# Kernel optimization log

Measured on AMD Instinct MI355X. Metric: run time of the kernel, lower is better.

The kernel has to match this reference:

```python
import jax, jax.numpy as jnp
import numpy as np

N = 50000      # nodes
E = 800000     # directed edges (avg degree 16 in/out pairs)
F_IN = 16      # dataset.num_features
H = 64         # neuron
S = 7          # Chebyshev order


def setup_inputs() -> dict:
    key = jax.random.key(0)
    ks = jax.random.split(key, 12)
    x = jax.random.normal(ks[0], (N, F_IN), dtype=jnp.float32)
    row = jax.random.randint(ks[1], (E,), 0, N, dtype=jnp.int32)
    off = jax.random.randint(ks[2], (E,), 1, N, dtype=jnp.int32)
    col = (row + off) % N  # guarantees no self-loops (PyG removes them)
    edge_index = jnp.stack([row, col])
    lambda_max = jnp.array([2.0], dtype=jnp.float32)
    def lin(k, fi, fo):
        return jax.random.normal(k, (S, fi, fo), dtype=jnp.float32) * (1.0 / np.sqrt(fi))
    W1 = lin(ks[3], F_IN, H); b1 = jnp.zeros((H,), jnp.float32)
    W2 = lin(ks[4], H, H);    b2 = jnp.zeros((H,), jnp.float32)
    W3 = lin(ks[5], H, H);    b3 = jnp.zeros((H,), jnp.float32)
    Wfc = jax.random.normal(ks[6], (H, 1), dtype=jnp.float32) * (1.0 / np.sqrt(H))
    bfc = jnp.zeros((1,), jnp.float32)
    return {"x": x, "edge_index": edge_index, "lambda_max": lambda_max,
            "W1": W1, "b1": b1, "W2": W2, "b2": b2, "W3": W3, "b3": b3,
            "Wfc": Wfc, "bfc": bfc}


def _make_spmv(edge_index, lam, n):
    # L_hat = 2/lambda_max * (I - D^-1/2 A D^-1/2) - I  (PyG ChebConv sym norm)
    row, col = edge_index[0], edge_index[1]
    deg = jax.ops.segment_sum(jnp.ones_like(row, dtype=jnp.float32), row, num_segments=n)
    dis = jnp.where(deg > 0, jax.lax.rsqrt(jnp.maximum(deg, 1.0)), 0.0)
    w = -(2.0 / lam) * dis[row] * dis[col]      # off-diagonal edge weights
    diag = 2.0 / lam - 1.0                       # self-loop weight
    def spmv(xx):  # L_hat @ xx
        return jax.ops.segment_sum(w[:, None] * xx[col], row, num_segments=n) + diag * xx
    return spmv


def _cheb(xx, W, b, spmv):
    Tx0 = xx
    out = Tx0 @ W[0]
    Tx1 = spmv(Tx0)
    out = out + Tx1 @ W[1]
    for k in range(2, W.shape[0]):  # fixed small S loop
        Tx2 = 2.0 * spmv(Tx1) - Tx0
        out = out + Tx2 @ W[k]
        Tx0, Tx1 = Tx1, Tx2
    return out + b


def reference(x, edge_index, lambda_max, W1, b1, W2, b2, W3, b3, Wfc, bfc):
    lam = lambda_max[0]
    spmv = _make_spmv(edge_index, lam, x.shape[0])
    h = jax.nn.relu(_cheb(x, W1, b1, spmv))
    h = jax.nn.relu(_cheb(h, W2, b2, spmv))
    h = jax.nn.relu(_cheb(h, W3, b3, spmv))
    return h @ Wfc + bfc
```

## Files before the change

### kernel.cpp

```cpp
#include <hip/hip_runtime.h>
#include <math.h>


#define WS_ALIGN(x) (((size_t)(x) + 255) & ~(size_t)255)

using f16x8 = __attribute__((ext_vector_type(8))) _Float16;
using f32x4 = __attribute__((ext_vector_type(4))) float;

__device__ inline float h2f_bits(unsigned int b) {
  unsigned short s = (unsigned short)(b & 0xffffu);
  _Float16 h;
  __builtin_memcpy(&h, &s, 2);
  return (float)h;
}
__device__ inline unsigned short f2h_bits(float f) {
  _Float16 h = (_Float16)f;
  unsigned short s;
  __builtin_memcpy(&s, &h, 2);
  return s;
}
union H4 {
  ushort4 u;
  _Float16 h[4];
};

__global__ __launch_bounds__(256) void hist_kernel(const int* __restrict__ row, int E,
                                                   int* __restrict__ deg) {
  int i = blockIdx.x * 256 + threadIdx.x;
  if (i < E) atomicAdd(&deg[row[i]], 1);
}

__global__ __launch_bounds__(256) void scan_sum_kernel(const int* __restrict__ deg,
                                                       int* __restrict__ bsum, int n) {
  int base = blockIdx.x * 1024 + threadIdx.x;
  int v = 0;
#pragma unroll
  for (int u = 0; u < 4; ++u) {
    int i = base + u * 256;
    if (i < n) v += deg[i];
  }
#pragma unroll
  for (int off = 32; off > 0; off >>= 1) v += __shfl_down(v, off, 64);
  __shared__ int ws[4];
  int lane = threadIdx.x & 63, wave = threadIdx.x >> 6;
  if (lane == 0) ws[wave] = v;
  __syncthreads();
  if (threadIdx.x == 0) bsum[blockIdx.x] = ws[0] + ws[1] + ws[2] + ws[3];
}

__global__ __launch_bounds__(64) void scan_bsum_kernel(int* __restrict__ bsum, int nb) {
  int t = threadIdx.x;
  int v = (t < nb) ? bsum[t] : 0;
  int sc = v;
#pragma unroll
  for (int off = 1; off < 64; off <<= 1) {
    int tv = __shfl_up(sc, off, 64);
    if (t >= off) sc += tv;
  }
  if (t < nb) bsum[t] = sc - v;
}

__global__ __launch_bounds__(256) void scan_out_kernel(const int* __restrict__ deg,
                                                       const int* __restrict__ bsum,
                                                       int* __restrict__ row_ptr,
                                                       int* __restrict__ cursor,
                                                       float* __restrict__ dis, int n) {
  int base = blockIdx.x * 1024 + threadIdx.x * 4;
  int loc[4];
  int s = 0;
#pragma unroll
  for (int u = 0; u < 4; ++u) {
    int i = base + u;
    loc[u] = (i < n) ? deg[i] : 0;
    s += loc[u];
  }
  int lane = threadIdx.x & 63, wave = threadIdx.x >> 6;
  int sc = s;
#pragma unroll
  for (int off = 1; off < 64; off <<= 1) {
    int tv = __shfl_up(sc, off, 64);
    if (lane >= off) sc += tv;
  }
  __shared__ int wtot[4];
  if (lane == 63) wtot[wave] = sc;
  __syncthreads();
  int pre = sc - s + bsum[blockIdx.x];
  for (int w = 0; w < wave; ++w) pre += wtot[w];
  if (blockIdx.x == 0 && threadIdx.x == 0) row_ptr[0] = 0;
  int running = pre;
#pragma unroll
  for (int u = 0; u < 4; ++u) {
    int i = base + u;
    if (i < n) {
      cursor[i] = running;
      dis[i] = (loc[u] > 0) ? (1.0f / sqrtf((float)loc[u])) : 0.0f;
      running += loc[u];
      row_ptr[i + 1] = running;
    }
  }
}

__global__ __launch_bounds__(256) void scatter_kernel(const int* __restrict__ row,
                                                      const int* __restrict__ col, int E,
                                                      int* __restrict__ cursor,
                                                      const float* __restrict__ dis,
                                                      const float* __restrict__ lamp,
                                                      unsigned int* __restrict__ cw) {
  int i = blockIdx.x * 256 + threadIdx.x;
  if (i >= E) return;
  int r = row[i], c = col[i];
  int pos = atomicAdd(&cursor[r], 1);
  float w = -(2.0f / lamp[0]) * dis[r] * dis[c];
  cw[pos] = ((unsigned int)c << 16) | (unsigned int)f2h_bits(w);
}

__global__ __launch_bounds__(256) void x_to_t1_kernel(const float* __restrict__ x,
                                                      ushort* __restrict__ T1, int n) {
  int j = blockIdx.x * 256 + threadIdx.x;
  if (j >= n * 8) return;
  int row = j >> 3, s = j & 7;
  if (s < 4) {
    float4 v = ((const float4*)x)[(size_t)row * 4 + s];
    ushort4 o;
    o.x = f2h_bits(v.x);
    o.y = f2h_bits(v.y);
    o.z = f2h_bits(v.z);
    o.w = f2h_bits(v.w);
    ((ushort4*)T1)[(size_t)row * 32 + s] = o;
  } else {
    ((ushort4*)T1)[(size_t)row * 32 + 28 + (s - 4)] = make_ushort4(0, 0, 0, 0);
  }
}

template <int KREAL, int KT>
__global__ __launch_bounds__(256) void wpk_prep(const float* __restrict__ W,
                                                ushort* __restrict__ Wpk) {
  int t = blockIdx.x * 256 + threadIdx.x;
  if (t >= KT * 256) return;
  int kt = t >> 8, nt = (t >> 6) & 3, l = t & 63;
  int col = nt * 16 + (l & 15);
  int kb = kt * 32 + ((l >> 4) << 3);
  ushort tmp[8];
#pragma unroll
  for (int j = 0; j < 8; ++j) {
    int k = kb + j;
    float v = (k < KREAL) ? W[(size_t)k * 64 + col] : 0.0f;
    tmp[j] = f2h_bits(v);
  }
  ushort4* dst = (ushort4*)Wpk + (size_t)((kt * 4 + nt) * 64 + l) * 2;
  dst[0] = make_ushort4(tmp[0], tmp[1], tmp[2], tmp[3]);
  dst[1] = make_ushort4(tmp[4], tmp[5], tmp[6], tmp[7]);
}

template <int F, int MODE, int S4>
__global__ __launch_bounds__(256) void spmv_pure(const int* __restrict__ row_ptr,
                                                 const unsigned int* __restrict__ cw,
                                                 const float* __restrict__ lamp,
                                                 const ushort4* __restrict__ xin,
                                                 const ushort4* __restrict__ sub,
                                                 ushort4* __restrict__ xout, int n) {
  constexpr int LPR = F / 4;
  constexpr int RPB = 256 / LPR;
  constexpr int EPL = 16 / LPR;
  int i = blockIdx.x * RPB + threadIdx.y;
  if (i >= n) return;
  int f4 = threadIdx.x;
  int lane = (threadIdx.y * LPR + f4) & 63;
  int grpbase = lane - f4;
  float diag = 2.0f / lamp[0] - 1.0f;
  H4 xd;
  xd.u = xin[(size_t)i * S4 + f4];
  float4 a = make_float4(diag * (float)xd.h[0], diag * (float)xd.h[1],
                         diag * (float)xd.h[2], diag * (float)xd.h[3]);
  int s = row_ptr[i], e = row_ptr[i + 1];

  for (int j0 = s; j0 < e; j0 += 16) {
    unsigned int pv[EPL];
#pragma unroll
    for (int u = 0; u < EPL; ++u) {
      int jj = j0 + f4 * EPL + u;
      pv[u] = cw[jj < e ? jj : (e - 1)];
    }
    H4 xv[16];
    float ww[16];
#pragma unroll
    for (int u = 0; u < 16; ++u) {
      unsigned int pu = (unsigned int)__shfl((int)pv[u % EPL], grpbase + u / EPL, 64);
      bool valid = (j0 + u) < e;
      ww[u] = valid ? h2f_bits(pu) : 0.0f;
      int ad = valid ? (int)(pu >> 16) : i;
      xv[u].u = xin[(size_t)ad * S4 + f4];
    }
#pragma unroll
    for (int u = 0; u < 16; ++u) {
      a.x += ww[u] * (float)xv[u].h[0];
      a.y += ww[u] * (float)xv[u].h[1];
      a.z += ww[u] * (float)xv[u].h[2];
      a.w += ww[u] * (float)xv[u].h[3];
    }
  }

  float4 r;
  if (MODE == 1) {
    H4 sv;
    sv.u = sub[(size_t)i * S4 + f4];
    r = make_float4(2.0f * a.x - (float)sv.h[0], 2.0f * a.y - (float)sv.h[1],
                    2.0f * a.z - (float)sv.h[2], 2.0f * a.w - (float)sv.h[3]);
  } else {
    r = a;
  }
  ushort4 o;
  o.x = f2h_bits(r.x);
  o.y = f2h_bits(r.y);
  o.z = f2h_bits(r.z);
  o.w = f2h_bits(r.w);
  xout[(size_t)i * S4 + f4] = o;
}

template <int KT, bool LAST>
__global__ __launch_bounds__(256) void gemm_mfma(const ushort* __restrict__ A,
                                                 const ushort* __restrict__ Wpk,
                                                 const float* __restrict__ bias,
                                                 ushort* __restrict__ dsth, int dstride,
                                                 float* __restrict__ dacc, int n) {
  int l = threadIdx.x & 63;
  int tile = blockIdx.x * 4 + (threadIdx.x >> 6);
  int r0 = tile * 16;
  if (r0 >= n) return;
  constexpr int ASTR = KT * 32;
  const f16x8* ap = (const f16x8*)(A + (size_t)(r0 + (l & 15)) * ASTR + ((l >> 4) << 3));
  const f16x8* bp = (const f16x8*)Wpk + l;
  f32x4 c[4] = {{0.f, 0.f, 0.f, 0.f},
                {0.f, 0.f, 0.f, 0.f},
                {0.f, 0.f, 0.f, 0.f},
                {0.f, 0.f, 0.f, 0.f}};
#pragma unroll
  for (int kt = 0; kt < KT; ++kt) {
    f16x8 af = ap[kt * 4];
#pragma unroll
    for (int nt = 0; nt < 4; ++nt) {
      f16x8 bf = bp[(kt * 4 + nt) * 64];
      c[nt] = __builtin_amdgcn_mfma_f32_16x16x32_f16(af, bf, c[nt], 0, 0, 0);
    }
  }
  int rb = r0 + ((l >> 4) << 2);
  int cc = l & 15;
#pragma unroll
  for (int nt = 0; nt < 4; ++nt) {
    int col = nt * 16 + cc;
    if (LAST) {
#pragma unroll
      for (int j = 0; j < 4; ++j) dacc[(size_t)(rb + j) * 64 + col] = c[nt][j];
    } else {
      float bv = bias[col];
#pragma unroll
      for (int j = 0; j < 4; ++j) {
        float v = fmaxf(c[nt][j] + bv, 0.0f);
        dsth[(size_t)(rb + j) * dstride + col] = f2h_bits(v);
      }
    }
  }
}

__global__ __launch_bounds__(256) void fc_fused_kernel(const float* __restrict__ acc,
                                                       const float* __restrict__ b,
                                                       const float* __restrict__ Wfc,
                                                       const float* __restrict__ bfc,
                                                       float* __restrict__ out, int n) {
  int i = blockIdx.x * 4 + threadIdx.y;
  if (i >= n) return;
  int l = threadIdx.x;
  float v = fmaxf(acc[(size_t)i * 64 + l] + b[l], 0.0f) * Wfc[l];
#pragma unroll
  for (int off = 32; off > 0; off >>= 1) v += __shfl_down(v, off, 64);
  if (l == 0) out[i] = v + bfc[0];
}

extern "C" void kernel_launch(void* const* d_in, const int* in_sizes, int n_in, void* d_out,
                              int out_size, void* d_ws, size_t ws_size, hipStream_t stream) {
  const float* x = (const float*)d_in[0];
  const int* ei = (const int*)d_in[1];
  const float* lamp = (const float*)d_in[2];
  const float* W1 = (const float*)d_in[3];
  const float* b1 = (const float*)d_in[4];
  const float* W2 = (const float*)d_in[5];
  const float* b2 = (const float*)d_in[6];
  const float* W3 = (const float*)d_in[7];
  const float* b3 = (const float*)d_in[8];
  const float* Wfc = (const float*)d_in[9];
  const float* bfc = (const float*)d_in[10];

  const int N = in_sizes[0] / 16;
  const int E = in_sizes[1] / 2;
  const int* row = ei;
  const int* col = ei + E;

  char* p = (char*)d_ws;
  auto alloc = [&](size_t bytes) {
    char* r = p;
    p += WS_ALIGN(bytes);
    return r;
  };
  int* deg = (int*)alloc((size_t)N * 4);
  int* row_ptr = (int*)alloc((size_t)(N + 1) * 4);
  int* cursor = (int*)alloc((size_t)N * 4);
  unsigned int* cw = (unsigned int*)alloc((size_t)E * 4);
  float* dis = (float*)alloc((size_t)N * 4);
  int* bsum = (int*)alloc(256 * 4);
  ushort* T1 = (ushort*)alloc((size_t)N * 128 * 2);
  ushort* TXC = (ushort*)alloc((size_t)N * 448 * 2);
  float* acc = (float*)alloc((size_t)N * 64 * 4);
  ushort* Wpk1 = (ushort*)alloc((size_t)4 * 256 * 8 * 2);
  ushort* Wpk2 = (ushort*)alloc((size_t)14 * 256 * 8 * 2);
  ushort* Wpk3 = (ushort*)alloc((size_t)14 * 256 * 8 * 2);
  (void)ws_size;
  (void)n_in;
  (void)out_size;

  hipMemsetAsync(deg, 0, (size_t)N * 4, stream);
  hist_kernel<<<(E + 255) / 256, 256, 0, stream>>>(row, E, deg);
  int nb = (N + 1023) / 1024;
  scan_sum_kernel<<<nb, 256, 0, stream>>>(deg, bsum, N);
  scan_bsum_kernel<<<1, 64, 0, stream>>>(bsum, nb);
  scan_out_kernel<<<nb, 256, 0, stream>>>(deg, bsum, row_ptr, cursor, dis, N);
  scatter_kernel<<<(E + 255) / 256, 256, 0, stream>>>(row, col, E, cursor, dis, lamp, cw);

  x_to_t1_kernel<<<(N * 8 + 255) / 256, 256, 0, stream>>>(x, T1, N);
  wpk_prep<112, 4><<<4, 256, 0, stream>>>(W1, Wpk1);
  wpk_prep<448, 14><<<14, 256, 0, stream>>>(W2, Wpk2);
  wpk_prep<448, 14><<<14, 256, 0, stream>>>(W3, Wpk3);

  {
    ushort4* B = (ushort4*)T1;
    dim3 bs(4, 64);
    int gs = (N + 63) / 64;
    spmv_pure<16, 0, 32><<<gs, bs, 0, stream>>>(row_ptr, cw, lamp, B + 0, nullptr, B + 4, N);
    for (int k = 2; k < 7; ++k)
      spmv_pure<16, 1, 32><<<gs, bs, 0, stream>>>(row_ptr, cw, lamp, B + 4 * (k - 1),
                                                  B + 4 * (k - 2), B + 4 * k, N);
    gemm_mfma<4, false><<<(N / 16 + 3) / 4 + 1, 256, 0, stream>>>(T1, Wpk1, b1, TXC, 448,
                                                                  nullptr, N);
  }

  for (int layer = 2; layer <= 3; ++layer) {
    ushort4* B = (ushort4*)TXC;
    dim3 bs(16, 16);
    int gs = (N + 15) / 16;
    spmv_pure<64, 0, 112><<<gs, bs, 0, stream>>>(row_ptr, cw, lamp, B + 0, nullptr, B + 16, N);
    for (int k = 2; k < 7; ++k)
      spmv_pure<64, 1, 112><<<gs, bs, 0, stream>>>(row_ptr, cw, lamp, B + 16 * (k - 1),
                                                   B + 16 * (k - 2), B + 16 * k, N);
    if (layer == 2)
      gemm_mfma<14, false><<<(N / 16 + 3) / 4 + 1, 256, 0, stream>>>(TXC, Wpk2, b2, TXC, 448,
                                                                     nullptr, N);
    else
      gemm_mfma<14, true><<<(N / 16 + 3) / 4 + 1, 256, 0, stream>>>(TXC, Wpk3, nullptr,
                                                                    nullptr, 0, acc, N);
  }

  fc_fused_kernel<<<(N + 3) / 4, dim3(64, 4), 0, stream>>>(acc, b3, Wfc, bfc, (float*)d_out,
                                                           N);
}
```

Measured before the change: 454.7 us.

## Split feature tensors into slot-major slices and bucket-sort CSR build

Reorganizes the Chebyshev basis buffers from row-interleaved layout into contiguous per-order slices, and runs the 64-wide layers as two 32-wide feature slices. Each SpMV gather then touches a compact array that fits cache better, at the cost of doubling the number of SpMV launches and re-reading the edge list twice. The CSR construction now scatters into 64-row buckets with per-bucket atomics, then sorts each bucket in LDS, replacing per-row global atomics. Nontemporal loads and stores are added for streamed edges and outputs.

```diff
diff --git a/kernel.cpp b/kernel.cpp
--- a/kernel.cpp
+++ b/kernel.cpp
@@ -22,6 +22,7 @@
 union H4 {
   ushort4 u;
   _Float16 h[4];
+  unsigned long long q;
 };
 
 __global__ __launch_bounds__(256) void hist_kernel(const int* __restrict__ row, int E,
@@ -63,7 +64,6 @@
 __global__ __launch_bounds__(256) void scan_out_kernel(const int* __restrict__ deg,
                                                        const int* __restrict__ bsum,
                                                        int* __restrict__ row_ptr,
-                                                       int* __restrict__ cursor,
                                                        float* __restrict__ dis, int n) {
   int base = blockIdx.x * 1024 + threadIdx.x * 4;
   int loc[4];
@@ -92,7 +92,6 @@
   for (int u = 0; u < 4; ++u) {
     int i = base + u;
     if (i < n) {
-      cursor[i] = running;
       dis[i] = (loc[u] > 0) ? (1.0f / sqrtf((float)loc[u])) : 0.0f;
       running += loc[u];
       row_ptr[i + 1] = running;
@@ -100,35 +99,69 @@
   }
 }
 
-__global__ __launch_bounds__(256) void scatter_kernel(const int* __restrict__ row,
-                                                      const int* __restrict__ col, int E,
-                                                      int* __restrict__ cursor,
-                                                      const float* __restrict__ dis,
-                                                      const float* __restrict__ lamp,
-                                                      unsigned int* __restrict__ cw) {
+__global__ __launch_bounds__(256) void bcur_init_kernel(const int* __restrict__ row_ptr,
+                                                        int* __restrict__ bcur, int nb) {
+  int b = blockIdx.x * 256 + threadIdx.x;
+  if (b < nb) bcur[b] = row_ptr[b * 64];
+}
+
+__global__ __launch_bounds__(256) void scatter_rc_kernel(const int* __restrict__ row,
+                                                         const int* __restrict__ col, int E,
+                                                         int* __restrict__ bcur,
+                                                         unsigned int* __restrict__ rc_stage) {
   int i = blockIdx.x * 256 + threadIdx.x;
   if (i >= E) return;
   int r = row[i], c = col[i];
-  int pos = atomicAdd(&cursor[r], 1);
-  float w = -(2.0f / lamp[0]) * dis[r] * dis[c];
-  cw[pos] = ((unsigned int)c << 16) | (unsigned int)f2h_bits(w);
-}
-
-__global__ __launch_bounds__(256) void x_to_t1_kernel(const float* __restrict__ x,
-                                                      ushort* __restrict__ T1, int n) {
-  int j = blockIdx.x * 256 + threadIdx.x;
-  if (j >= n * 8) return;
-  int row = j >> 3, s = j & 7;
-  if (s < 4) {
-    float4 v = ((const float4*)x)[(size_t)row * 4 + s];
+  int pos = atomicAdd(&bcur[r >> 6], 1);
+  rc_stage[pos] = ((unsigned int)r << 16) | (unsigned int)c;
+}
+
+__global__ __launch_bounds__(256) void bucket_finalize_kernel(
+    const int* __restrict__ row_ptr, const unsigned int* __restrict__ rc_stage,
+    const float* __restrict__ dis, const float* __restrict__ lamp,
+    unsigned int* __restrict__ cw, int n) {
+  __shared__ int lcur[64];
+  __shared__ unsigned int lcw[4096];
+  int r0 = blockIdx.x * 64;
+  int r1 = min(r0 + 64, n);
+  int base = row_ptr[r0];
+  int cnt = row_ptr[r1] - base;
+  int t = threadIdx.x;
+  if (t < r1 - r0) lcur[t] = row_ptr[r0 + t] - base;
+  __syncthreads();
+  float sc = -(2.0f / lamp[0]);
+  bool fits = (cnt <= 4096);
+  for (int j = t; j < cnt; j += 256) {
+    unsigned int e = rc_stage[base + j];
+    int r = (int)(e >> 16), c = (int)(e & 0xffffu);
+    float w = sc * dis[r] * dis[c];
+    unsigned int val = ((unsigned int)c << 16) | (unsigned int)f2h_bits(w);
+    int p = atomicAdd(&lcur[r - r0], 1);
+    if (fits)
+      lcw[p] = val;
+    else
+      cw[base + p] = val;
+  }
+  __syncthreads();
+  if (fits)
+    for (int j = t; j < cnt; j += 256) cw[base + j] = lcw[j];
+}
+
+__global__ __launch_bounds__(256) void x_to_slots_kernel(const float* __restrict__ x,
+                                                         ushort* __restrict__ T1, int n) {
+  int t = blockIdx.x * 256 + threadIdx.x;
+  if (t < n * 4) {
+    int row = t >> 2, q = t & 3;
+    float4 v = ((const float4*)x)[(size_t)row * 4 + q];
     ushort4 o;
     o.x = f2h_bits(v.x);
     o.y = f2h_bits(v.y);
     o.z = f2h_bits(v.z);
     o.w = f2h_bits(v.w);
-    ((ushort4*)T1)[(size_t)row * 32 + s] = o;
-  } else {
-    ((ushort4*)T1)[(size_t)row * 32 + 28 + (s - 4)] = make_ushort4(0, 0, 0, 0);
+    ((ushort4*)T1)[(size_t)row * 4 + q] = o;
+  } else if (t < n * 8) {
+    int t2 = t - n * 4;
+    ((ushort4*)(T1 + (size_t)7 * n * 16))[t2] = make_ushort4(0, 0, 0, 0);
   }
 }
 
@@ -152,14 +185,14 @@
   dst[1] = make_ushort4(tmp[4], tmp[5], tmp[6], tmp[7]);
 }
 
-template <int F, int MODE, int S4>
-__global__ __launch_bounds__(256) void spmv_pure(const int* __restrict__ row_ptr,
-                                                 const unsigned int* __restrict__ cw,
-                                                 const float* __restrict__ lamp,
-                                                 const ushort4* __restrict__ xin,
-                                                 const ushort4* __restrict__ sub,
-                                                 ushort4* __restrict__ xout, int n) {
-  constexpr int LPR = F / 4;
+template <int SW, int MODE>
+__global__ __launch_bounds__(256) void spmv_slice(const int* __restrict__ row_ptr,
+                                                  const unsigned int* __restrict__ cw,
+                                                  const float* __restrict__ lamp,
+                                                  const ushort4* __restrict__ xin,
+                                                  const ushort4* __restrict__ sub,
+                                                  ushort4* __restrict__ xout, int n) {
+  constexpr int LPR = SW / 4;
   constexpr int RPB = 256 / LPR;
   constexpr int EPL = 16 / LPR;
   int i = blockIdx.x * RPB + threadIdx.y;
@@ -169,7 +202,7 @@
   int grpbase = lane - f4;
   float diag = 2.0f / lamp[0] - 1.0f;
   H4 xd;
-  xd.u = xin[(size_t)i * S4 + f4];
+  xd.u = xin[(size_t)i * LPR + f4];
   float4 a = make_float4(diag * (float)xd.h[0], diag * (float)xd.h[1],
                          diag * (float)xd.h[2], diag * (float)xd.h[3]);
   int s = row_ptr[i], e = row_ptr[i + 1];
@@ -179,7 +212,7 @@
 #pragma unroll
     for (int u = 0; u < EPL; ++u) {
       int jj = j0 + f4 * EPL + u;
-      pv[u] = cw[jj < e ? jj : (e - 1)];
+      pv[u] = __builtin_nontemporal_load(&cw[jj < e ? jj : (e - 1)]);
     }
     H4 xv[16];
     float ww[16];
@@ -189,7 +222,7 @@
       bool valid = (j0 + u) < e;
       ww[u] = valid ? h2f_bits(pu) : 0.0f;
       int ad = valid ? (int)(pu >> 16) : i;
-      xv[u].u = xin[(size_t)ad * S4 + f4];
+      xv[u].u = xin[(size_t)ad * LPR + f4];
     }
 #pragma unroll
     for (int u = 0; u < 16; ++u) {
@@ -203,32 +236,32 @@
   float4 r;
   if (MODE == 1) {
     H4 sv;
-    sv.u = sub[(size_t)i * S4 + f4];
+    sv.q = __builtin_nontemporal_load((const unsigned long long*)&sub[(size_t)i * LPR + f4]);
     r = make_float4(2.0f * a.x - (float)sv.h[0], 2.0f * a.y - (float)sv.h[1],
                     2.0f * a.z - (float)sv.h[2], 2.0f * a.w - (float)sv.h[3]);
   } else {
     r = a;
   }
-  ushort4 o;
-  o.x = f2h_bits(r.x);
-  o.y = f2h_bits(r.y);
-  o.z = f2h_bits(r.z);
-  o.w = f2h_bits(r.w);
-  xout[(size_t)i * S4 + f4] = o;
-}
-
-template <int KT, bool LAST>
+  H4 o;
+  o.u.x = f2h_bits(r.x);
+  o.u.y = f2h_bits(r.y);
+  o.u.z = f2h_bits(r.z);
+  o.u.w = f2h_bits(r.w);
+  __builtin_nontemporal_store(o.q, (unsigned long long*)&xout[(size_t)i * LPR + f4]);
+}
+
+template <int SW, int KT, bool LAST>
 __global__ __launch_bounds__(256) void gemm_mfma(const ushort* __restrict__ A,
                                                  const ushort* __restrict__ Wpk,
                                                  const float* __restrict__ bias,
-                                                 ushort* __restrict__ dsth, int dstride,
+                                                 ushort* __restrict__ dsth,
                                                  float* __restrict__ dacc, int n) {
   int l = threadIdx.x & 63;
   int tile = blockIdx.x * 4 + (threadIdx.x >> 6);
   int r0 = tile * 16;
   if (r0 >= n) return;
-  constexpr int ASTR = KT * 32;
-  const f16x8* ap = (const f16x8*)(A + (size_t)(r0 + (l & 15)) * ASTR + ((l >> 4) << 3));
+  size_t slotsz = (size_t)n * SW;
+  int row = r0 + (l & 15);
   const f16x8* bp = (const f16x8*)Wpk + l;
   f32x4 c[4] = {{0.f, 0.f, 0.f, 0.f},
                 {0.f, 0.f, 0.f, 0.f},
@@ -236,7 +269,15 @@
                 {0.f, 0.f, 0.f, 0.f}};
 #pragma unroll
   for (int kt = 0; kt < KT; ++kt) {
-    f16x8 af = ap[kt * 4];
+    int slot, off;
+    if constexpr (SW == 32) {
+      slot = kt;
+      off = (l >> 4) << 3;
+    } else {
+      slot = 2 * kt + ((l >> 4) >> 1);
+      off = ((l >> 4) & 1) << 3;
+    }
+    f16x8 af = *(const f16x8*)(A + slot * slotsz + (size_t)row * SW + off);
 #pragma unroll
     for (int nt = 0; nt < 4; ++nt) {
       f16x8 bf = bp[(kt * 4 + nt) * 64];
@@ -245,6 +286,7 @@
   }
   int rb = r0 + ((l >> 4) << 2);
   int cc = l & 15;
+  size_t dslot = (size_t)n * 32;
 #pragma unroll
   for (int nt = 0; nt < 4; ++nt) {
     int col = nt * 16 + cc;
@@ -253,10 +295,11 @@
       for (int j = 0; j < 4; ++j) dacc[(size_t)(rb + j) * 64 + col] = c[nt][j];
     } else {
       float bv = bias[col];
+      ushort* dbase = dsth + (col >> 5) * dslot + (col & 31);
 #pragma unroll
       for (int j = 0; j < 4; ++j) {
         float v = fmaxf(c[nt][j] + bv, 0.0f);
-        dsth[(size_t)(rb + j) * dstride + col] = f2h_bits(v);
+        dbase[(size_t)(rb + j) * 32] = f2h_bits(v);
       }
     }
   }
@@ -303,12 +346,13 @@
   };
   int* deg = (int*)alloc((size_t)N * 4);
   int* row_ptr = (int*)alloc((size_t)(N + 1) * 4);
-  int* cursor = (int*)alloc((size_t)N * 4);
+  int* bcur = (int*)alloc((size_t)((N + 63) / 64) * 4);
   unsigned int* cw = (unsigned int*)alloc((size_t)E * 4);
+  unsigned int* rc_stage = (unsigned int*)alloc((size_t)E * 4);
   float* dis = (float*)alloc((size_t)N * 4);
   int* bsum = (int*)alloc(256 * 4);
-  ushort* T1 = (ushort*)alloc((size_t)N * 128 * 2);
-  ushort* TXC = (ushort*)alloc((size_t)N * 448 * 2);
+  ushort* T1 = (ushort*)alloc((size_t)8 * N * 16 * 2);
+  ushort* TXC = (ushort*)alloc((size_t)14 * N * 32 * 2);
   float* acc = (float*)alloc((size_t)N * 64 * 4);
   ushort* Wpk1 = (ushort*)alloc((size_t)4 * 256 * 8 * 2);
   ushort* Wpk2 = (ushort*)alloc((size_t)14 * 256 * 8 * 2);
@@ -317,45 +361,53 @@
   (void)n_in;
   (void)out_size;
 
-  hipMemsetAsync(deg, 0, (size_t)N * 4, stream);
+  const int NB = (N + 63) / 64;
+
+  (void)hipMemsetAsync(deg, 0, (size_t)N * 4, stream);
   hist_kernel<<<(E + 255) / 256, 256, 0, stream>>>(row, E, deg);
   int nb = (N + 1023) / 1024;
   scan_sum_kernel<<<nb, 256, 0, stream>>>(deg, bsum, N);
   scan_bsum_kernel<<<1, 64, 0, stream>>>(bsum, nb);
-  scan_out_kernel<<<nb, 256, 0, stream>>>(deg, bsum, row_ptr, cursor, dis, N);
-  scatter_kernel<<<(E + 255) / 256, 256, 0, stream>>>(row, col, E, cursor, dis, lamp, cw);
-
-  x_to_t1_kernel<<<(N * 8 + 255) / 256, 256, 0, stream>>>(x, T1, N);
+  scan_out_kernel<<<nb, 256, 0, stream>>>(deg, bsum, row_ptr, dis, N);
+  bcur_init_kernel<<<(NB + 255) / 256, 256, 0, stream>>>(row_ptr, bcur, NB);
+  scatter_rc_kernel<<<(E + 255) / 256, 256, 0, stream>>>(row, col, E, bcur, rc_stage);
+  bucket_finalize_kernel<<<NB, 256, 0, stream>>>(row_ptr, rc_stage, dis, lamp, cw, N);
+
+  x_to_slots_kernel<<<(N * 8 + 255) / 256, 256, 0, stream>>>(x, T1, N);
   wpk_prep<112, 4><<<4, 256, 0, stream>>>(W1, Wpk1);
   wpk_prep<448, 14><<<14, 256, 0, stream>>>(W2, Wpk2);
   wpk_prep<448, 14><<<14, 256, 0, stream>>>(W3, Wpk3);
 
   {
-    ushort4* B = (ushort4*)T1;
+    size_t ssz = (size_t)N * 16;
+    auto S = [&](int k) { return (ushort4*)(T1 + (size_t)k * ssz); };
     dim3 bs(4, 64);
     int gs = (N + 63) / 64;
-    spmv_pure<16, 0, 32><<<gs, bs, 0, stream>>>(row_ptr, cw, lamp, B + 0, nullptr, B + 4, N);
+    spmv_slice<16, 0><<<gs, bs, 0, stream>>>(row_ptr, cw, lamp, S(0), nullptr, S(1), N);
     for (int k = 2; k < 7; ++k)
-      spmv_pure<16, 1, 32><<<gs, bs, 0, stream>>>(row_ptr, cw, lamp, B + 4 * (k - 1),
-                                                  B + 4 * (k - 2), B + 4 * k, N);
-    gemm_mfma<4, false><<<(N / 16 + 3) / 4 + 1, 256, 0, stream>>>(T1, Wpk1, b1, TXC, 448,
-                                                                  nullptr, N);
+      spmv_slice<16, 1><<<gs, bs, 0, stream>>>(row_ptr, cw, lamp, S(k - 1), S(k - 2), S(k), N);
+    gemm_mfma<16, 4, false><<<(N / 16 + 3) / 4 + 1, 256, 0, stream>>>(T1, Wpk1, b1, TXC,
+                                                                      nullptr, N);
   }
 
   for (int layer = 2; layer <= 3; ++layer) {
-    ushort4* B = (ushort4*)TXC;
-    dim3 bs(16, 16);
-    int gs = (N + 15) / 16;
-    spmv_pure<64, 0, 112><<<gs, bs, 0, stream>>>(row_ptr, cw, lamp, B + 0, nullptr, B + 16, N);
-    for (int k = 2; k < 7; ++k)
-      spmv_pure<64, 1, 112><<<gs, bs, 0, stream>>>(row_ptr, cw, lamp, B + 16 * (k - 1),
-                                                   B + 16 * (k - 2), B + 16 * k, N);
+    size_t ssz = (size_t)N * 32;
+    auto S = [&](int k, int s) { return (ushort4*)(TXC + (size_t)(2 * k + s) * ssz); };
+    dim3 bs(8, 32);
+    int gs = (N + 31) / 32;
+    for (int s = 0; s < 2; ++s) {
+      spmv_slice<32, 0><<<gs, bs, 0, stream>>>(row_ptr, cw, lamp, S(0, s), nullptr, S(1, s),
+                                               N);
+      for (int k = 2; k < 7; ++k)
+        spmv_slice<32, 1><<<gs, bs, 0, stream>>>(row_ptr, cw, lamp, S(k - 1, s), S(k - 2, s),
+                                                 S(k, s), N);
+    }
     if (layer == 2)
-      gemm_mfma<14, false><<<(N / 16 + 3) / 4 + 1, 256, 0, stream>>>(TXC, Wpk2, b2, TXC, 448,
-                                                                     nullptr, N);
+      gemm_mfma<32, 14, false><<<(N / 16 + 3) / 4 + 1, 256, 0, stream>>>(TXC, Wpk2, b2, TXC,
+                                                                         nullptr, N);
     else
-      gemm_mfma<14, true><<<(N / 16 + 3) / 4 + 1, 256, 0, stream>>>(TXC, Wpk3, nullptr,
-                                                                    nullptr, 0, acc, N);
+      gemm_mfma<32, 14, true><<<(N / 16 + 3) / 4 + 1, 256, 0, stream>>>(TXC, Wpk3, nullptr,
+                                                                        nullptr, acc, N);
   }
 
   fc_fused_kernel<<<(N + 3) / 4, dim3(64, 4), 0, stream>>>(acc, b3, Wfc, bfc, (float*)d_out,
```

New measurement: 698.6 us. 1.54x slower.
